# Optimization experiments

Hardware: AMD Instinct MI355X
Metric: run time of the kernel (lower is better)

## Reference

```python
import jax, jax.numpy as jnp
import numpy as np

DIM = 1024
N_HEADS = 16
HEAD_DIM = DIM // N_HEADS
B, N, M = 2, 2048, 2048


def setup_inputs() -> dict:
    key = jax.random.key(0)
    ks = jax.random.split(key, 10)
    s = 1.0 / np.sqrt(DIM)
    return {
        "x1": jax.random.normal(ks[0], (B, N, DIM), dtype=jnp.float32),
        "x2": jax.random.normal(ks[1], (B, M, DIM), dtype=jnp.float32),
        "Wq": jax.random.normal(ks[2], (DIM, DIM), dtype=jnp.float32) * s,
        "bq": jnp.zeros((DIM,), dtype=jnp.float32),
        "Wk": jax.random.normal(ks[3], (DIM, DIM), dtype=jnp.float32) * s,
        "bk": jnp.zeros((DIM,), dtype=jnp.float32),
        "Wv": jax.random.normal(ks[4], (DIM, DIM), dtype=jnp.float32) * s,
        "bv": jnp.zeros((DIM,), dtype=jnp.float32),
        "Wo": jax.random.normal(ks[5], (DIM, DIM), dtype=jnp.float32) * s,
        "bo": jnp.zeros((DIM,), dtype=jnp.float32),
    }


def reference(x1, x2, Wq, bq, Wk, bk, Wv, bv, Wo, bo):
    b, n, _ = x1.shape
    m = x2.shape[1]
    # projections (Linear: x @ W^T + b)
    q = x1 @ Wq.T + bq  # [b, n, dim]
    k = x2 @ Wk.T + bk  # [b, m, dim]
    v = x2 @ Wv.T + bv  # [b, m, dim]
    # split heads -> [b, h, seq, head_dim]
    q = q.reshape(b, n, N_HEADS, HEAD_DIM).transpose(0, 2, 1, 3)
    k = k.reshape(b, m, N_HEADS, HEAD_DIM).transpose(0, 2, 1, 3)
    v = v.reshape(b, m, N_HEADS, HEAD_DIM).transpose(0, 2, 1, 3)
    scale = 1.0 / jnp.sqrt(jnp.asarray(HEAD_DIM, dtype=q.dtype))
    scores = jnp.einsum('bhnd,bhmd->bhnm', q, k) * scale  # [b, h, n, m]
    attn = jax.nn.softmax(scores, axis=-1)
    o = jnp.einsum('bhnm,bhmd->bhnd', attn, v)  # [b, h, n, head_dim]
    o = o.transpose(0, 2, 1, 3).reshape(b, n, DIM)  # merge heads
    return o @ Wo.T + bo
```

## Files before the change

### kernel.cpp

```cpp
#include <hip/hip_runtime.h>
#include <stdint.h>

typedef unsigned short u16;
typedef __attribute__((ext_vector_type(4))) float f32x4;
typedef __attribute__((ext_vector_type(16))) float f32x16;
typedef __attribute__((ext_vector_type(8))) __bf16 bf16x8;
typedef __attribute__((ext_vector_type(8))) unsigned short u16x8;
typedef __attribute__((ext_vector_type(4))) unsigned short u16x4;

#define DIM_    1024
#define NHEADS_ 16
#define HD_     64
#define BB_     2
#define NN_     2048
#define MM_     2048

#define QSCALE 0.180336884f

__device__ inline u16 f32_to_bf16u(float f) {
  union { float f; uint32_t u; } x; x.f = f;
  uint32_t r = x.u + 0x7FFFu + ((x.u >> 16) & 1u);
  return (u16)(r >> 16);
}

__device__ inline void gload_lds16(const u16* g, u16* l) {
  u16* gnc = const_cast<u16*>(g);
  __builtin_amdgcn_global_load_lds(
      (__attribute__((address_space(1))) void*)gnc,
      (__attribute__((address_space(3))) void*)l, 16, 0, 0);
}

__device__ inline uint32_t cvt_pk_bf16(float lo, float hi) {
  uint32_t r;
  asm("v_cvt_pk_bf16_f32 %0, %1, %2" : "=v"(r) : "v"(lo), "v"(hi));
  return r;
}
__device__ inline void permlane32_swap(uint32_t& a, uint32_t& b) {
  asm("v_permlane32_swap_b32 %0, %1" : "+v"(a), "+v"(b));
}

__global__ void cast_all(const float* s0, u16* d0, const float* s1, u16* d1,
                         const float* s2, u16* d2, const float* s3, u16* d3,
                         const float* s4, u16* d4, const float* s5, u16* d5) {
  const float* s; u16* d; int n4;
  switch (blockIdx.y) {
    case 0: s = s0; d = d0; n4 = (BB_ * NN_ * DIM_) / 4; break;
    case 1: s = s1; d = d1; n4 = (BB_ * MM_ * DIM_) / 4; break;
    case 2: s = s2; d = d2; n4 = (DIM_ * DIM_) / 4; break;
    case 3: s = s3; d = d3; n4 = (DIM_ * DIM_) / 4; break;
    case 4: s = s4; d = d4; n4 = (DIM_ * DIM_) / 4; break;
    default: s = s5; d = d5; n4 = (DIM_ * DIM_) / 4; break;
  }
  int stride = gridDim.x * blockDim.x;
  for (int i = blockIdx.x * blockDim.x + threadIdx.x; i < n4; i += stride) {
    float4 f = reinterpret_cast<const float4*>(s)[i];
    u16x4 u;
    u.x = f32_to_bf16u(f.x);
    u.y = f32_to_bf16u(f.y);
    u.z = f32_to_bf16u(f.z);
    u.w = f32_to_bf16u(f.w);
    reinterpret_cast<u16x4*>(d)[i] = u;
  }
}

#define BM 128
#define BN 128
#define BK 64

template <bool BF16OUT>
__device__ __forceinline__
void gemm_body(const u16* __restrict__ A, const u16* __restrict__ Bm,
               const float* __restrict__ bias, void* __restrict__ Cout,
               int M, int N, int K, float scale,
               u16* As , u16* Bs ) {
  const int tid  = threadIdx.x;
  const int lane = tid & 63;
  const int wid  = tid >> 6;
  const int wr = wid >> 2, wc = wid & 3;
  const int fr = lane & 15, fq = lane >> 4;
  const int bm = blockIdx.x, bn = blockIdx.y;
  const int lrow = lane >> 3;
  const int scol = (((lane & 7) ^ lrow) * 8);

  f32x4 acc[4][2];
  #pragma unroll
  for (int m = 0; m < 4; ++m)
    #pragma unroll
    for (int n = 0; n < 2; ++n)
      acc[m][n] = f32x4{0.f, 0.f, 0.f, 0.f};

  const int NT = K / BK;

  auto stage = [&](int buf, int t) {
    int k0 = t * BK;
    #pragma unroll
    for (int c = 0; c < 2; ++c) {
      int ch  = wid * 2 + c;
      int row = ch * 8 + lrow;
      gload_lds16(A  + (size_t)(bm * BM + row) * K + k0 + scol, &As[buf * BM * BK + ch * 512]);
      gload_lds16(Bm + (size_t)(bn * BN + row) * K + k0 + scol, &Bs[buf * BN * BK + ch * 512]);
    }
  };

  stage(0, 0);
  __syncthreads();
  int cur = 0;
  for (int t = 0; t < NT; ++t) {
    if (t + 1 < NT) stage(cur ^ 1, t + 1);
    #pragma unroll
    for (int ks = 0; ks < 2; ++ks) {
      bf16x8 af[4], bfr[2];
      #pragma unroll
      for (int m = 0; m < 4; ++m)
        af[m] = *reinterpret_cast<const bf16x8*>(
            &As[cur * BM * BK + (wr * 64 + m * 16 + fr) * BK + (((ks * 4 + fq) ^ (fr & 7)) * 8)]);
      #pragma unroll
      for (int n = 0; n < 2; ++n)
        bfr[n] = *reinterpret_cast<const bf16x8*>(
            &Bs[cur * BN * BK + (wc * 32 + n * 16 + fr) * BK + (((ks * 4 + fq) ^ (fr & 7)) * 8)]);
      __builtin_amdgcn_s_setprio(1);
      #pragma unroll
      for (int m = 0; m < 4; ++m)
        #pragma unroll
        for (int n = 0; n < 2; ++n)
          acc[m][n] = __builtin_amdgcn_mfma_f32_16x16x32_bf16(af[m], bfr[n], acc[m][n], 0, 0, 0);
      __builtin_amdgcn_s_setprio(0);
    }
    __syncthreads();
    cur ^= 1;
  }

  #pragma unroll
  for (int n = 0; n < 2; ++n) {
    int col = bn * BN + wc * 32 + n * 16 + fr;
    float bv = bias[col];
    #pragma unroll
    for (int m = 0; m < 4; ++m) {
      #pragma unroll
      for (int i = 0; i < 4; ++i) {
        int row = bm * BM + wr * 64 + m * 16 + fq * 4 + i;
        float v = (acc[m][n][i] + bv) * scale;
        if (BF16OUT)
          ((u16*)Cout)[(size_t)row * N + col] = f32_to_bf16u(v);
        else
          ((float*)Cout)[(size_t)row * N + col] = v;
      }
    }
  }
}

#define BK2 32

__global__ __launch_bounds__(512)
void gemm_qkv(const u16* __restrict__ x1b, const u16* __restrict__ x2b,
              const u16* __restrict__ Wqb, const float* __restrict__ bq, u16* qb,
              const u16* __restrict__ Wkb, const float* __restrict__ bk, u16* kb,
              const u16* __restrict__ Wvb, const float* __restrict__ bv, u16* vb) {
  __shared__ __align__(16) u16 As[2 * BM * BK2];
  __shared__ __align__(16) u16 Bs[2 * BN * BK2];
  const u16* A; const u16* W; const float* bias; u16* C; float scale;
  switch (blockIdx.z) {
    case 0:  A = x1b; W = Wqb; bias = bq; C = qb; scale = QSCALE; break;
    case 1:  A = x2b; W = Wkb; bias = bk; C = kb; scale = 1.0f;   break;
    default: A = x2b; W = Wvb; bias = bv; C = vb; scale = 1.0f;   break;
  }
  const int K = DIM_;
  const int tid  = threadIdx.x;
  const int lane = tid & 63;
  const int wid  = tid >> 6;
  const int wr = wid >> 2, wc = wid & 3;
  const int fr = lane & 15, fq = lane >> 4;
  const int bm = blockIdx.x, bn = blockIdx.y;

  const int srow = tid >> 2;
  const int sch  = tid & 3;
  const int scol = ((sch ^ ((srow >> 1) & 3)) * 8);
  const int rsw  = (fr >> 1) & 3;

  f32x4 acc[4][2];
  #pragma unroll
  for (int m = 0; m < 4; ++m)
    #pragma unroll
    for (int n = 0; n < 2; ++n)
      acc[m][n] = f32x4{0.f, 0.f, 0.f, 0.f};

  const int NT = K / BK2;

  auto stage = [&](int buf, int t) {
    int k0 = t * BK2;
    gload_lds16(A + (size_t)(bm * BM + srow) * K + k0 + scol, &As[buf * BM * BK2 + tid * 8]);
    gload_lds16(W + (size_t)(bn * BN + srow) * K + k0 + scol, &Bs[buf * BN * BK2 + tid * 8]);
  };

  stage(0, 0);
  __syncthreads();
  int cur = 0;
  for (int t = 0; t < NT; ++t) {
    if (t + 1 < NT) stage(cur ^ 1, t + 1);
    bf16x8 af[4], bfr[2];
    #pragma unroll
    for (int m = 0; m < 4; ++m)
      af[m] = *reinterpret_cast<const bf16x8*>(
          &As[cur * BM * BK2 + (wr * 64 + m * 16 + fr) * BK2 + ((fq ^ rsw) * 8)]);
    #pragma unroll
    for (int n = 0; n < 2; ++n)
      bfr[n] = *reinterpret_cast<const bf16x8*>(
          &Bs[cur * BN * BK2 + (wc * 32 + n * 16 + fr) * BK2 + ((fq ^ rsw) * 8)]);
    __builtin_amdgcn_s_setprio(1);
    #pragma unroll
    for (int m = 0; m < 4; ++m)
      #pragma unroll
      for (int n = 0; n < 2; ++n)
        acc[m][n] = __builtin_amdgcn_mfma_f32_16x16x32_bf16(af[m], bfr[n], acc[m][n], 0, 0, 0);
    __builtin_amdgcn_s_setprio(0);
    __syncthreads();
    cur ^= 1;
  }

  #pragma unroll
  for (int n = 0; n < 2; ++n) {
    int col = bn * BN + wc * 32 + n * 16 + fr;
    float bv = bias[col];
    #pragma unroll
    for (int m = 0; m < 4; ++m) {
      #pragma unroll
      for (int i = 0; i < 4; ++i) {
        int row = bm * BM + wr * 64 + m * 16 + fq * 4 + i;
        float v = (acc[m][n][i] + bv) * scale;
        C[(size_t)row * DIM_ + col] = f32_to_bf16u(v);
      }
    }
  }
}

__global__ __launch_bounds__(512)
void gemm_o(const u16* __restrict__ A, const u16* __restrict__ W,
            const float* __restrict__ bias, float* __restrict__ C) {
  __shared__ __align__(16) u16 As[2 * BM * BK];
  __shared__ __align__(16) u16 Bs[2 * BN * BK];
  gemm_body<false>(A, W, bias, C, BB_ * NN_, DIM_, DIM_, 1.0f, As, Bs);
}

#define QB 128
#define KVB 64

__global__ __launch_bounds__(512)
void attn_fwd(const u16* __restrict__ qg, const u16* __restrict__ kg,
              const u16* __restrict__ vg, u16* __restrict__ og) {
  __shared__ __align__(16) u16 KVs[6 * KVB * HD_];
  const int tid = threadIdx.x, lane = tid & 63, wid = tid >> 6;
  const int hi = lane >> 5;
  const int l31 = lane & 31;
  const int wq = wid >> 1, wk = wid & 1;

  int lin = blockIdx.x + gridDim.x * (blockIdx.y + gridDim.y * blockIdx.z);
  int xcd = lin & 7, slot = lin >> 3;
  int r = slot & 15, gg2 = slot >> 4;
  int g = xcd + 8 * gg2;
  int h = g & 15, b = g >> 4;

  const size_t base_q  = (size_t)b * NN_ * DIM_ + (size_t)h * HD_;
  const size_t base_kv = (size_t)b * MM_ * DIM_ + (size_t)h * HD_;
  const int lrow = lane >> 3;
  const int scol = (((lane & 7) ^ lrow) * 8);

  bf16x8 qf[4];
  const int qrow = r * QB + wq * 32 + l31;
  #pragma unroll
  for (int step = 0; step < 4; ++step)
    qf[step] = *reinterpret_cast<const bf16x8*>(
        qg + base_q + (size_t)qrow * DIM_ + step * 16 + hi * 8);

  bf16x8 onesf;
  #pragma unroll
  for (int j = 0; j < 8; ++j) onesf[j] = (__bf16)1.0f;

  f32x16 oacc[2];
  #pragma unroll
  for (int dgrp = 0; dgrp < 2; ++dgrp)
    #pragma unroll
    for (int rg = 0; rg < 16; ++rg) oacc[dgrp][rg] = 0.f;
  f32x16 lacc;
  #pragma unroll
  for (int rg = 0; rg < 16; ++rg) lacc[rg] = 0.f;

  const int NT = MM_ / KVB;

  auto stageK = [&](int buf, int t) {
    int kv0 = t * KVB;
    int row = wid * 8 + lrow;
    gload_lds16(kg + base_kv + (size_t)(kv0 + row) * DIM_ + scol,
                &KVs[buf * 4096 + wid * 512]);
  };
  auto loadV = [&](int t, u16x8& vpre) {
    int kv0 = t * KVB;
    vpre = *reinterpret_cast<const u16x8*>(vg + base_kv + (size_t)(kv0 + lane) * DIM_ + wid * 8);
  };
  auto writeVT = [&](int buf, const u16x8& vpre) {
    #pragma unroll
    for (int j = 0; j < 8; ++j)
      KVs[(3 + buf) * 4096 + (wid * 8 + j) * KVB + (((lane >> 3) ^ j) * 8) + (lane & 7)] = vpre[j];
  };

  union PB { uint32_t w[4]; bf16x8 v; };

  auto compute = [&](int buf) {
    const u16* Kb = &KVs[buf * 4096];
    const u16* Vb = &KVs[(3 + buf) * 4096];
    f32x16 s;
    #pragma unroll
    for (int rg = 0; rg < 16; ++rg) s[rg] = 0.f;
    __builtin_amdgcn_s_setprio(1);
    #pragma unroll
    for (int step = 0; step < 4; ++step) {
      bf16x8 kf = *reinterpret_cast<const bf16x8*>(
          (const char*)Kb + (wk * 32 + l31) * 128 + (((step * 2 + hi) ^ (lane & 7)) * 16));
      s = __builtin_amdgcn_mfma_f32_32x32x16_bf16(kf, qf[step], s, 0, 0, 0);
    }
    __builtin_amdgcn_s_setprio(0);

    float p[16];
    #pragma unroll
    for (int rg = 0; rg < 16; ++rg) p[rg] = __builtin_amdgcn_exp2f(s[rg]);

    PB pb[2];
    #pragma unroll
    for (int u = 0; u < 2; ++u) {
      uint32_t x0 = cvt_pk_bf16(p[u * 8 + 0], p[u * 8 + 1]);
      uint32_t y0 = cvt_pk_bf16(p[u * 8 + 4], p[u * 8 + 5]);
      permlane32_swap(x0, y0);
      uint32_t x1 = cvt_pk_bf16(p[u * 8 + 2], p[u * 8 + 3]);
      uint32_t y1 = cvt_pk_bf16(p[u * 8 + 6], p[u * 8 + 7]);
      permlane32_swap(x1, y1);
      pb[u].w[0] = x0; pb[u].w[1] = x1; pb[u].w[2] = y0; pb[u].w[3] = y1;
    }

    __builtin_amdgcn_s_setprio(1);
    #pragma unroll
    for (int u = 0; u < 2; ++u)
      lacc = __builtin_amdgcn_mfma_f32_32x32x16_bf16(onesf, pb[u].v, lacc, 0, 0, 0);
    #pragma unroll
    for (int dgrp = 0; dgrp < 2; ++dgrp)
      #pragma unroll
      for (int u = 0; u < 2; ++u) {
        bf16x8 vf = *reinterpret_cast<const bf16x8*>(
            (const char*)Vb + (dgrp * 32 + l31) * 128 +
            (((wk * 4 + u * 2 + hi) ^ (lane & 7)) * 16));
        oacc[dgrp] = __builtin_amdgcn_mfma_f32_32x32x16_bf16(vf, pb[u].v, oacc[dgrp], 0, 0, 0);
      }
    __builtin_amdgcn_s_setprio(0);
  };

  {
    u16x8 v0, v1;
    loadV(0, v0);
    loadV(1, v1);
    stageK(0, 0);
    stageK(1, 1);
    writeVT(0, v0);
    writeVT(1, v1);
    __syncthreads();
  }

  int cur = 0, stg = 2;
  for (int t = 0; t < NT; ++t) {
    u16x8 vpre;
    bool pre = (t + 2 < NT);
    if (pre) {
      loadV(t + 2, vpre);
      stageK(stg, t + 2);
    }
    compute(cur);
    if (pre) writeVT(stg, vpre);
    __syncthreads();
    cur = (cur == 2) ? 0 : cur + 1;
    stg = (stg == 2) ? 0 : stg + 1;
  }

  float* Od = (float*)&KVs[0];
  float* Ls = (float*)&KVs[0] + 128 * 65;
  u16*  Of  = (u16*)&KVs[0];

  if (wk == 1) {
    #pragma unroll
    for (int dgrp = 0; dgrp < 2; ++dgrp)
      #pragma unroll
      for (int rg = 0; rg < 16; ++rg) {
        int d = dgrp * 32 + (rg & 3) + 8 * (rg >> 2) + 4 * hi;
        Od[(wq * 32 + l31) * 65 + d] = oacc[dgrp][rg];
      }
    if (hi == 0) Ls[wq * 32 + l31] = lacc[0];
  }
  __syncthreads();
  if (wk == 0) {
    float inv = 1.f / (lacc[0] + Ls[wq * 32 + l31]);
    #pragma unroll
    for (int dgrp = 0; dgrp < 2; ++dgrp)
      #pragma unroll
      for (int rg = 0; rg < 16; ++rg) {
        int d = dgrp * 32 + (rg & 3) + 8 * (rg >> 2) + 4 * hi;
        oacc[dgrp][rg] = (oacc[dgrp][rg] + Od[(wq * 32 + l31) * 65 + d]) * inv;
      }
  }
  __syncthreads();
  if (wk == 0) {
    #pragma unroll
    for (int dgrp = 0; dgrp < 2; ++dgrp)
      #pragma unroll
      for (int rg = 0; rg < 16; ++rg) {
        int d = dgrp * 32 + (rg & 3) + 8 * (rg >> 2) + 4 * hi;
        Of[(wq * 32 + l31) * 68 + d] = f32_to_bf16u(oacc[dgrp][rg]);
      }
  }
  __syncthreads();
  #pragma unroll
  for (int itr = 0; itr < 2; ++itr) {
    int idx = itr * 512 + tid;
    int qq = idx >> 3;
    int ck = idx & 7;
    u16x8 v = *reinterpret_cast<const u16x8*>(&Of[qq * 68 + ck * 8]);
    *reinterpret_cast<u16x8*>(og + base_q + (size_t)(r * QB + qq) * DIM_ + ck * 8) = v;
  }
}

extern "C" void kernel_launch(void* const* d_in, const int* in_sizes, int n_in,
                              void* d_out, int out_size, void* d_ws, size_t ws_size,
                              hipStream_t stream) {
  (void)in_sizes; (void)n_in; (void)out_size; (void)ws_size;
  const float* x1 = (const float*)d_in[0];
  const float* x2 = (const float*)d_in[1];
  const float* Wq = (const float*)d_in[2];
  const float* bq = (const float*)d_in[3];
  const float* Wk = (const float*)d_in[4];
  const float* bk = (const float*)d_in[5];
  const float* Wv = (const float*)d_in[6];
  const float* bv = (const float*)d_in[7];
  const float* Wo = (const float*)d_in[8];
  const float* bo = (const float*)d_in[9];
  float* out = (float*)d_out;

  char* ws = (char*)d_ws;
  u16* x1b = (u16*)(ws);
  u16* x2b = (u16*)(ws + (8u  << 20));
  u16* Wqb = (u16*)(ws + (16u << 20));
  u16* Wkb = (u16*)(ws + (18u << 20));
  u16* Wvb = (u16*)(ws + (20u << 20));
  u16* Wob = (u16*)(ws + (22u << 20));
  u16* qb  = (u16*)(ws + (24u << 20));
  u16* kb  = (u16*)(ws + (32u << 20));
  u16* vb  = (u16*)(ws + (40u << 20));
  u16* ob  = (u16*)(ws + (48u << 20));

  cast_all<<<dim3(512, 6), 256, 0, stream>>>(x1, x1b, x2, x2b, Wq, Wqb,
                                             Wk, Wkb, Wv, Wvb, Wo, Wob);

  const int Mrows = BB_ * NN_;
  dim3 gqkv(Mrows / BM, DIM_ / BN, 3);
  gemm_qkv<<<gqkv, 512, 0, stream>>>(x1b, x2b, Wqb, bq, qb, Wkb, bk, kb, Wvb, bv, vb);

  dim3 ga(NN_ / QB, NHEADS_, BB_);
  attn_fwd<<<ga, 512, 0, stream>>>(qb, kb, vb, ob);

  dim3 gg(Mrows / BM, DIM_ / BN);
  gemm_o<<<gg, 512, 0, stream>>>(ob, Wob, bo, out);
}
```

Before: 115.2 us.

## Write V transposed from QKV GEMM and stage it via async LDS loads

The V projection epilogue now transposes its tile through shared memory and writes V as [batch, dim, seq], so each head's V^T is contiguous along the sequence. The attention kernel then loads V^T tiles straight into LDS with the same direct global-to-LDS path used for K. This replaces the register load plus scalar scattered LDS transpose writes inside the main loop. In exchange the GEMM epilogue for the V slice gains an extra LDS round trip and a barrier.

```diff
diff --git a/kernel.cpp b/kernel.cpp
--- a/kernel.cpp
+++ b/kernel.cpp
@@ -155,14 +155,15 @@
 void gemm_qkv(const u16* __restrict__ x1b, const u16* __restrict__ x2b,
               const u16* __restrict__ Wqb, const float* __restrict__ bq, u16* qb,
               const u16* __restrict__ Wkb, const float* __restrict__ bk, u16* kb,
-              const u16* __restrict__ Wvb, const float* __restrict__ bv, u16* vb) {
-  __shared__ __align__(16) u16 As[2 * BM * BK2];
-  __shared__ __align__(16) u16 Bs[2 * BN * BK2];
-  const u16* A; const u16* W; const float* bias; u16* C; float scale;
+              const u16* __restrict__ Wvb, const float* __restrict__ bv, u16* vbT) {
+  __shared__ __align__(16) u16 SMEM[16896];
+  u16* As = SMEM;
+  u16* Bs = SMEM + 2 * BM * BK2;
+  const u16* A; const u16* W; const float* bias; float scale;
   switch (blockIdx.z) {
-    case 0:  A = x1b; W = Wqb; bias = bq; C = qb; scale = QSCALE; break;
-    case 1:  A = x2b; W = Wkb; bias = bk; C = kb; scale = 1.0f;   break;
-    default: A = x2b; W = Wvb; bias = bv; C = vb; scale = 1.0f;   break;
+    case 0:  A = x1b; W = Wqb; bias = bq; scale = QSCALE; break;
+    case 1:  A = x2b; W = Wkb; bias = bk; scale = 1.0f;   break;
+    default: A = x2b; W = Wvb; bias = bv; scale = 1.0f;   break;
   }
   const int K = DIM_;
   const int tid  = threadIdx.x;
@@ -217,18 +218,47 @@
     cur ^= 1;
   }
 
-  #pragma unroll
-  for (int n = 0; n < 2; ++n) {
-    int col = bn * BN + wc * 32 + n * 16 + fr;
-    float bv = bias[col];
-    #pragma unroll
-    for (int m = 0; m < 4; ++m) {
-      #pragma unroll
-      for (int i = 0; i < 4; ++i) {
-        int row = bm * BM + wr * 64 + m * 16 + fq * 4 + i;
-        float v = (acc[m][n][i] + bv) * scale;
-        C[(size_t)row * DIM_ + col] = f32_to_bf16u(v);
-      }
+  if (blockIdx.z != 2) {
+    u16* C = (blockIdx.z == 0) ? qb : kb;
+    #pragma unroll
+    for (int n = 0; n < 2; ++n) {
+      int col = bn * BN + wc * 32 + n * 16 + fr;
+      float bv = bias[col];
+      #pragma unroll
+      for (int m = 0; m < 4; ++m) {
+        #pragma unroll
+        for (int i = 0; i < 4; ++i) {
+          int row = bm * BM + wr * 64 + m * 16 + fq * 4 + i;
+          float v = (acc[m][n][i] + bv) * scale;
+          C[(size_t)row * DIM_ + col] = f32_to_bf16u(v);
+        }
+      }
+    }
+  } else {
+    #pragma unroll
+    for (int n = 0; n < 2; ++n) {
+      int col = wc * 32 + n * 16 + fr;
+      float bv = bias[bn * BN + col];
+      #pragma unroll
+      for (int m = 0; m < 4; ++m) {
+        #pragma unroll
+        for (int i = 0; i < 4; ++i) {
+          int row = wr * 64 + m * 16 + fq * 4 + i;
+          SMEM[col * 132 + row] = f32_to_bf16u(acc[m][n][i] + bv);
+        }
+      }
+    }
+    __syncthreads();
+    const int bb = bm >> 4;
+    const int mmb = (bm & 15) * 128;
+    #pragma unroll
+    for (int itr = 0; itr < 4; ++itr) {
+      int idx = itr * 512 + tid;
+      int dl = idx >> 4;
+      int ck = idx & 15;
+      u16x8 v = *reinterpret_cast<const u16x8*>(&SMEM[dl * 132 + ck * 8]);
+      *reinterpret_cast<u16x8*>(
+          vbT + ((size_t)bb * 1024 + bn * BN + dl) * (size_t)MM_ + mmb + ck * 8) = v;
     }
   }
 }
@@ -246,7 +276,7 @@
 
 __global__ __launch_bounds__(512)
 void attn_fwd(const u16* __restrict__ qg, const u16* __restrict__ kg,
-              const u16* __restrict__ vg, u16* __restrict__ og) {
+              const u16* __restrict__ vtg, u16* __restrict__ og) {
   __shared__ __align__(16) u16 KVs[6 * KVB * HD_];
   const int tid = threadIdx.x, lane = tid & 63, wid = tid >> 6;
   const int hi = lane >> 5;
@@ -261,6 +291,7 @@
 
   const size_t base_q  = (size_t)b * NN_ * DIM_ + (size_t)h * HD_;
   const size_t base_kv = (size_t)b * MM_ * DIM_ + (size_t)h * HD_;
+  const size_t base_vt = ((size_t)b * 1024 + (size_t)h * HD_) * (size_t)MM_;
   const int lrow = lane >> 3;
   const int scol = (((lane & 7) ^ lrow) * 8);
 
@@ -292,14 +323,12 @@
     gload_lds16(kg + base_kv + (size_t)(kv0 + row) * DIM_ + scol,
                 &KVs[buf * 4096 + wid * 512]);
   };
-  auto loadV = [&](int t, u16x8& vpre) {
+  auto stageVT = [&](int buf, int t) {
     int kv0 = t * KVB;
-    vpre = *reinterpret_cast<const u16x8*>(vg + base_kv + (size_t)(kv0 + lane) * DIM_ + wid * 8);
-  };
-  auto writeVT = [&](int buf, const u16x8& vpre) {
-    #pragma unroll
-    for (int j = 0; j < 8; ++j)
-      KVs[(3 + buf) * 4096 + (wid * 8 + j) * KVB + (((lane >> 3) ^ j) * 8) + (lane & 7)] = vpre[j];
+    int row = wid * 8 + lrow;
+    int scol2 = (((lane & 7) ^ (row & 7)) * 8);
+    gload_lds16(vtg + base_vt + (size_t)row * MM_ + kv0 + scol2,
+                &KVs[(3 + buf) * 4096 + wid * 512]);
   };
 
   union PB { uint32_t w[4]; bf16x8 v; };
@@ -351,27 +380,17 @@
     __builtin_amdgcn_s_setprio(0);
   };
 
-  {
-    u16x8 v0, v1;
-    loadV(0, v0);
-    loadV(1, v1);
-    stageK(0, 0);
-    stageK(1, 1);
-    writeVT(0, v0);
-    writeVT(1, v1);
-    __syncthreads();
-  }
+  stageK(0, 0); stageVT(0, 0);
+  stageK(1, 1); stageVT(1, 1);
+  __syncthreads();
 
   int cur = 0, stg = 2;
   for (int t = 0; t < NT; ++t) {
-    u16x8 vpre;
-    bool pre = (t + 2 < NT);
-    if (pre) {
-      loadV(t + 2, vpre);
+    if (t + 2 < NT) {
       stageK(stg, t + 2);
+      stageVT(stg, t + 2);
     }
     compute(cur);
-    if (pre) writeVT(stg, vpre);
     __syncthreads();
     cur = (cur == 2) ? 0 : cur + 1;
     stg = (stg == 2) ? 0 : stg + 1;
@@ -448,7 +467,7 @@
   u16* Wob = (u16*)(ws + (22u << 20));
   u16* qb  = (u16*)(ws + (24u << 20));
   u16* kb  = (u16*)(ws + (32u << 20));
-  u16* vb  = (u16*)(ws + (40u << 20));
+  u16* vbT = (u16*)(ws + (40u << 20));
   u16* ob  = (u16*)(ws + (48u << 20));
 
   cast_all<<<dim3(512, 6), 256, 0, stream>>>(x1, x1b, x2, x2b, Wq, Wqb,
@@ -456,10 +475,10 @@
 
   const int Mrows = BB_ * NN_;
   dim3 gqkv(Mrows / BM, DIM_ / BN, 3);
-  gemm_qkv<<<gqkv, 512, 0, stream>>>(x1b, x2b, Wqb, bq, qb, Wkb, bk, kb, Wvb, bv, vb);
+  gemm_qkv<<<gqkv, 512, 0, stream>>>(x1b, x2b, Wqb, bq, qb, Wkb, bk, kb, Wvb, bv, vbT);
 
   dim3 ga(NN_ / QB, NHEADS_, BB_);
-  attn_fwd<<<ga, 512, 0, stream>>>(qb, kb, vb, ob);
+  attn_fwd<<<ga, 512, 0, stream>>>(qb, kb, vbT, ob);
 
   dim3 gg(Mrows / BM, DIM_ / BN);
   gemm_o<<<gg, 512, 0, stream>>>(ob, Wob, bo, out);
```

Measured after the change: 112.5 us. -2.4%, faster.
